# Kernel tuning notes

Measured on AMD Instinct MI355X. Metric: run time of the kernel, lower is better.

Reference implementation:

```python
import jax, jax.numpy as jnp
import numpy as np

ALPHA = 0.2  # LeakyReLU negative slope

def setup_inputs() -> dict:
    key = jax.random.key(0)
    k1, k2, k3 = jax.random.split(key, 3)
    B, N, Fin, Fout = 8, 2048, 256, 128
    h = jax.random.normal(k1, (B, N, Fin), dtype=jnp.float32)
    W = jax.random.normal(k2, (Fin, Fout), dtype=jnp.float32) * (1.414 / np.sqrt(Fin))
    a = jax.random.normal(k3, (2 * Fout, 1), dtype=jnp.float32) * 0.1
    return {"h": h, "W": W, "a": a}

def reference(h, W, a):
    # Wh: [B, N, D]
    Wh = jnp.einsum('bni,io->bno', h, W)
    D = Wh.shape[-1]
    a1 = a[:D, 0]   # weights for the 'i' (repeat_interleave) half
    a2 = a[D:, 0]   # weights for the 'j' (repeat) half
    s1 = Wh @ a1    # [B, N]
    s2 = Wh @ a2    # [B, N]
    # e[b,i,j] = leakyrelu(s1[b,i] + s2[b,j])  (fused form of the O(N^2*2D) concat)
    e = s1[:, :, None] + s2[:, None, :]
    e = jnp.where(e >= 0, e, ALPHA * e)
    # original applies softmax over dim=1 (the i axis)
    attention = jax.nn.softmax(e, axis=1)
    # dropout is identity in eval mode
    h_prime = jnp.einsum('bij,bjd->bid', attention, Wh)
    # concat=True -> ELU
    return jax.nn.elu(h_prime)
```

## Files before the change

### kernel.cpp

```cpp
#include <hip/hip_runtime.h>
#include <hip/hip_bf16.h>


#define ALPHA 0.2f
#define LOG2E 1.4426950408889634f
constexpr int Bb=8, Nn=2048, FIN=256, FOUT=128;

typedef __attribute__((ext_vector_type(8))) short short8;
typedef __attribute__((ext_vector_type(4))) float f32x4;
typedef const __attribute__((address_space(1))) unsigned int* gptr_t;
typedef __attribute__((address_space(3))) unsigned int* lptr_t;

__device__ __forceinline__ float lrelu(float x){ return fmaxf(x, ALPHA*x); }
__device__ __forceinline__ unsigned short bfbits(float x){
    __hip_bfloat16 h = __float2bfloat16(x);
    return *(unsigned short*)&h;
}

__global__ __launch_bounds__(256) void k_prep(const float* __restrict__ W,
                                              __hip_bfloat16* __restrict__ WTt){
    const int idx = blockIdx.x*256 + threadIdx.x;
    #pragma unroll
    for (int v = 0; v < 4; ++v){
        const int widx = idx + v*8192;
        const int kk = widx & 31, n = (widx>>5)&127, kt = widx>>12;
        WTt[widx] = __float2bfloat16(W[(kt*32+kk)*FOUT + n]);
    }
}

__global__ __launch_bounds__(256) void k_wh(const float* __restrict__ h,
                                            const float* __restrict__ a,
                                            const __hip_bfloat16* __restrict__ WTt,
                                            float* __restrict__ s1,
                                            float* __restrict__ s2,
                                            __hip_bfloat16* __restrict__ WhT){
    const int blk = blockIdx.x;
    const int rowbase = blk * 32;
    const int b = blk >> 6;
    const int jt = (rowbase & (Nn-1)) >> 5;
    const int t = threadIdx.x;
    const int wave = t>>6, lane = t&63;
    const int wm = wave & 1, wn = wave >> 1;
    const int lm = lane & 15, q = lane >> 4;

    __shared__ __align__(16) float hs[32*260];
    __shared__ unsigned short tt[FOUT*40];
    __shared__ float s1red[2][32], s2red[2][32];

    {
        const float* srcbase = h + (size_t)rowbase*FIN;
        #pragma unroll
        for (int c = 0; c < 8; ++c){
            const int row = wave*8 + c;
            __builtin_amdgcn_global_load_lds(
                (gptr_t)(srcbase + (size_t)row*FIN + lane*4),
                (lptr_t)&hs[row*260], 16, 0, 0);
        }
    }
    __syncthreads();

    f32x4 acc[4];
    #pragma unroll
    for (int ntl = 0; ntl < 4; ++ntl) acc[ntl] = (f32x4){0.f,0.f,0.f,0.f};

    const float* hrow = &hs[(wm*16 + lm)*260];
    const short* Wt = (const short*)WTt;
    #pragma unroll
    for (int kt = 0; kt < 8; ++kt){
        float av[8];
        *(float4*)&av[0] = *(const float4*)&hrow[kt*32 + q*8];
        *(float4*)&av[4] = *(const float4*)&hrow[kt*32 + q*8 + 4];
        short8 afr;
        #pragma unroll
        for (int e = 0; e < 8; ++e) afr[e] = (short)bfbits(av[e]);
        #pragma unroll
        for (int ntl = 0; ntl < 4; ++ntl){
            const short8 bfr = *(const short8*)(Wt + ((kt*128 + wn*64 + ntl*16 + lm)*32 + q*8));
            acc[ntl] = __builtin_amdgcn_mfma_f32_16x16x32_bf16(afr, bfr, acc[ntl], 0,0,0);
        }
    }

    {
        float a1v[4], a2v[4];
        #pragma unroll
        for (int ntl = 0; ntl < 4; ++ntl){
            a1v[ntl] = a[wn*64 + ntl*16 + lm];
            a2v[ntl] = a[FOUT + wn*64 + ntl*16 + lm];
        }
        #pragma unroll
        for (int rg = 0; rg < 4; ++rg){
            float p1 = 0.f, p2 = 0.f;
            #pragma unroll
            for (int ntl = 0; ntl < 4; ++ntl){
                p1 += acc[ntl][rg]*a1v[ntl];
                p2 += acc[ntl][rg]*a2v[ntl];
            }
            #pragma unroll
            for (int m = 1; m < 16; m <<= 1){
                p1 += __shfl_xor(p1, m);
                p2 += __shfl_xor(p2, m);
            }
            if (lm == 0){
                s1red[wn][wm*16 + q*4 + rg] = p1;
                s2red[wn][wm*16 + q*4 + rg] = p2;
            }
        }
    }

    #pragma unroll
    for (int ntl = 0; ntl < 4; ++ntl){
        ushort4 u;
        u.x = bfbits(acc[ntl][0]); u.y = bfbits(acc[ntl][1]);
        u.z = bfbits(acc[ntl][2]); u.w = bfbits(acc[ntl][3]);
        *(ushort4*)&tt[(wn*64 + ntl*16 + lm)*40 + wm*16 + q*4] = u;
    }
    __syncthreads();

    if (t < 32){
        s1[rowbase + t] = (s1red[0][t] + s1red[1][t]) * LOG2E;
        s2[rowbase + t] = (s2red[0][t] + s2red[1][t]) * LOG2E;
    }
    {
        const int d = t >> 1, jh = (t & 1) * 16;
        const unsigned short* src = &tt[d*40 + jh];
        short8 v0 = *(const short8*)src;
        short8 v1 = *(const short8*)(src + 8);
        const int lmw = d & 15, ntw = d >> 4, q0 = (t & 1) * 2;
        const int u0 = (lmw & 7) + 8*(q0*16 + ntw*2 + (lmw >> 3));
        short* Wo = (short*)WhT;
        const size_t tb = ((size_t)(b*64 + jt))*4096;
        *(short8*)&Wo[tb + (size_t)u0*8]       = v0;
        *(short8*)&Wo[tb + (size_t)(u0+128)*8] = v1;
    }
}

__global__ __launch_bounds__(256) void k_z(const float* __restrict__ s1,
                                           const float* __restrict__ s2,
                                           float* __restrict__ l2z){
    const int b  = blockIdx.x >> 6;
    const int jt = blockIdx.x & 63;
    const int t  = threadIdx.x;
    const int jj = t & 31, part = t >> 5;
    const int j  = jt*32 + jj;
    __shared__ float s1s[Nn];
    __shared__ float red[8][33];

    {
        const float4* g = (const float4*)(s1 + (size_t)b*Nn);
        float4* p = (float4*)s1s;
        #pragma unroll
        for (int v0 = 0; v0 < 2; ++v0){ const int v = t + v0*256; p[v] = g[v]; }
    }
    __syncthreads();
    const float s2j = s2[b*Nn + j];
    float sum = 0.f;
    const float4* s4 = (const float4*)&s1s[part*256];
    #pragma unroll 4
    for (int v = 0; v < 64; ++v){
        float x[4]; *(float4*)x = s4[v];
        sum += __builtin_amdgcn_exp2f(lrelu(x[0]+s2j))
             + __builtin_amdgcn_exp2f(lrelu(x[1]+s2j))
             + __builtin_amdgcn_exp2f(lrelu(x[2]+s2j))
             + __builtin_amdgcn_exp2f(lrelu(x[3]+s2j));
    }
    red[part][jj] = sum;
    __syncthreads();
    if (part == 0){
        float Z = 0.f;
        #pragma unroll
        for (int p = 0; p < 8; ++p) Z += red[p][jj];
        l2z[b*Nn + j] = -__builtin_amdgcn_logf(Z);
    }
}

__global__ __launch_bounds__(256, 2) void k_pv(const float* __restrict__ s1,
                                               const float* __restrict__ s2,
                                               const float* __restrict__ l2z,
                                               const __hip_bfloat16* __restrict__ WhT,
                                               float* __restrict__ out){
    const int blk   = blockIdx.x;
    const int b     = blk & 7;
    const int ibase = (blk >> 3) * 32;
    const int t     = threadIdx.x;
    const int wave  = t >> 6, lane = t & 63;
    const int wm = wave & 1, kh = wave >> 1;
    const int lm = lane & 15, q = lane >> 4;

    __shared__ float s2s[Nn], lzs[Nn];
    __shared__ unsigned short Bs[2][2][8192];

    {
        const float4* g1 = (const float4*)(s2  + (size_t)b*Nn);
        const float4* g2 = (const float4*)(l2z + (size_t)b*Nn);
        float4* p1 = (float4*)s2s; float4* p2 = (float4*)lzs;
        #pragma unroll
        for (int v0 = 0; v0 < 2; ++v0){
            const int v = t + v0*256;
            p1[v] = g1[v]; p2[v] = g2[v];
        }
    }

    const float s1a = s1[(size_t)b*Nn + ibase + wm*16 + lm];

    f32x4 acc[8];
    #pragma unroll
    for (int nt = 0; nt < 8; ++nt) acc[nt] = (f32x4){0.f,0.f,0.f,0.f};

    const char* WtbB = (const char*)WhT + (size_t)b*64*8192;
    const int laneoff = wm*8192 + lane*16;
    const int dsbase  = (lm & 7)*16 + (lm >> 3)*128 + q*2048;

    {
        const char* src = WtbB + (size_t)(kh*16)*16384 + laneoff;
        unsigned short* dst = &Bs[0][kh][wm*4096];
        #pragma unroll
        for (int c = 0; c < 8; ++c)
            __builtin_amdgcn_global_load_lds((gptr_t)(src + c*1024),
                                             (lptr_t)(dst + c*512), 16, 0, 0);
    }

    int buf = 0;
    for (int it = 0; it < 16; ++it){
        __syncthreads();
        if (it + 1 < 16){
            const char* src = WtbB + (size_t)(kh*16 + it + 1)*16384 + laneoff;
            unsigned short* dst = &Bs[buf^1][kh][wm*4096];
            #pragma unroll
            for (int c = 0; c < 8; ++c)
                __builtin_amdgcn_global_load_lds((gptr_t)(src + c*1024),
                                                 (lptr_t)(dst + c*512), 16, 0, 0);
        }
        #pragma unroll
        for (int s = 0; s < 2; ++s){
            const char* tile = (const char*)&Bs[buf][kh][s*4096];
            short8 bfr[8];
            #pragma unroll
            for (int nt = 0; nt < 8; ++nt)
                bfr[nt] = *(const short8*)(tile + dsbase + nt*256);

            const int jb = (kh*16 + it)*64 + s*32 + q*8;
            float sarr[8], larr[8];
            *(float4*)&sarr[0] = *(const float4*)&s2s[jb];
            *(float4*)&sarr[4] = *(const float4*)&s2s[jb+4];
            *(float4*)&larr[0] = *(const float4*)&lzs[jb];
            *(float4*)&larr[4] = *(const float4*)&lzs[jb+4];
            short8 afa;
            #pragma unroll
            for (int e = 0; e < 8; ++e){
                const float z = s1a + sarr[e];
                afa[e] = (short)bfbits(__builtin_amdgcn_exp2f(fmaxf(z, ALPHA*z) + larr[e]));
            }
            #pragma unroll
            for (int nt = 0; nt < 8; ++nt)
                acc[nt] = __builtin_amdgcn_mfma_f32_16x16x32_bf16(afa, bfr[nt], acc[nt], 0,0,0);
        }
        buf ^= 1;
    }

    __syncthreads();
    float* comb = (float*)&Bs[0][0][0];
    if (kh == 0){
        #pragma unroll
        for (int nt = 0; nt < 8; ++nt)
            #pragma unroll
            for (int rg = 0; rg < 4; ++rg)
                comb[(wm*16 + q*4 + rg)*132 + nt*16 + lm] = acc[nt][rg];
    }
    __syncthreads();
    if (kh == 1){
        #pragma unroll
        for (int nt = 0; nt < 8; ++nt){
            const int col = nt*16 + lm;
            #pragma unroll
            for (int rg = 0; rg < 4; ++rg){
                const int row = wm*16 + q*4 + rg;
                const float x = acc[nt][rg] + comb[row*132 + col];
                out[((size_t)(b*Nn + ibase + row))*FOUT + col] = x > 0.f ? x : expm1f(x);
            }
        }
    }
}

extern "C" void kernel_launch(void* const* d_in, const int* in_sizes, int n_in,
                              void* d_out, int out_size, void* d_ws, size_t ws_size,
                              hipStream_t stream) {
    (void)in_sizes; (void)n_in; (void)out_size; (void)ws_size;
    const float* h = (const float*)d_in[0];
    const float* W = (const float*)d_in[1];
    const float* a = (const float*)d_in[2];
    float* out = (float*)d_out;

    float* ws    = (float*)d_ws;
    float* s1    = ws;
    float* s2    = s1 + Bb*Nn;
    float* l2z   = s2 + Bb*Nn;
    __hip_bfloat16* WTt = (__hip_bfloat16*)(l2z + Bb*Nn);
    __hip_bfloat16* WhT = WTt + 32768;

    k_prep<<<dim3(32),        dim3(256), 0, stream>>>(W, WTt);
    k_wh  <<<dim3(Bb*Nn/32),  dim3(256), 0, stream>>>(h, a, WTt, s1, s2, WhT);
    k_z   <<<dim3(Bb*64),     dim3(256), 0, stream>>>(s1, s2, l2z);
    k_pv  <<<dim3(Bb*Nn/32),  dim3(256), 0, stream>>>(s1, s2, l2z, WhT, out);
}
```

Baseline: 103.9 us.

## Switch attention-PV kernel to 32x32x16 MFMA with larger row tiles

Rewrites the final P·V kernel to use 32x32x16 bf16 MFMA instead of 16x16x32. Each block now covers 64 rows with 512 threads and a 4-way K split, and k_wh writes WhT in a matching swizzled layout. The aim is to compute fewer exponentials per useful FLOP, since each exp result feeds a bigger MFMA, and to load WhT tiles less often across blocks. The cost is a three-stage LDS reduction across the four K-split waves, larger shared memory use, and half as many blocks, which may lower occupancy.

New measurement: 100.1 us, median of 2. -3.7%, faster.

```diff
diff --git a/kernel.cpp b/kernel.cpp
--- a/kernel.cpp
+++ b/kernel.cpp
@@ -8,6 +8,7 @@
 
 typedef __attribute__((ext_vector_type(8))) short short8;
 typedef __attribute__((ext_vector_type(4))) float f32x4;
+typedef __attribute__((ext_vector_type(16))) float f32x16;
 typedef const __attribute__((address_space(1))) unsigned int* gptr_t;
 typedef __attribute__((address_space(3))) unsigned int* lptr_t;
 
@@ -121,16 +122,17 @@
         s2[rowbase + t] = (s2red[0][t] + s2red[1][t]) * LOG2E;
     }
     {
-        const int d = t >> 1, jh = (t & 1) * 16;
-        const unsigned short* src = &tt[d*40 + jh];
+        const int d = t >> 1, jsub16 = t & 1;
+        const unsigned short* src = &tt[d*40 + jsub16*16];
         short8 v0 = *(const short8*)src;
         short8 v1 = *(const short8*)(src + 8);
-        const int lmw = d & 15, ntw = d >> 4, q0 = (t & 1) * 2;
-        const int u0 = (lmw & 7) + 8*(q0*16 + ntw*2 + (lmw >> 3));
+        const int s  = (jt & 1)*2 + jsub16;
+        const int nt = d >> 5, col = d & 31;
+        const int u0 = (s*4 + nt)*64 + col;
         short* Wo = (short*)WhT;
-        const size_t tb = ((size_t)(b*64 + jt))*4096;
-        *(short8*)&Wo[tb + (size_t)u0*8]       = v0;
-        *(short8*)&Wo[tb + (size_t)(u0+128)*8] = v1;
+        const size_t tb = ((size_t)(b*32 + (jt >> 1)))*8192;
+        *(short8*)&Wo[tb + (size_t)u0*8]      = v0;
+        *(short8*)&Wo[tb + (size_t)(u0+32)*8] = v1;
     }
 }
 
@@ -173,46 +175,43 @@
     }
 }
 
-__global__ __launch_bounds__(256, 2) void k_pv(const float* __restrict__ s1,
+__global__ __launch_bounds__(512, 2) void k_pv(const float* __restrict__ s1,
                                                const float* __restrict__ s2,
                                                const float* __restrict__ l2z,
                                                const __hip_bfloat16* __restrict__ WhT,
                                                float* __restrict__ out){
     const int blk   = blockIdx.x;
     const int b     = blk & 7;
-    const int ibase = (blk >> 3) * 32;
+    const int ibase = (blk >> 3) * 64;
     const int t     = threadIdx.x;
     const int wave  = t >> 6, lane = t & 63;
-    const int wm = wave & 1, kh = wave >> 1;
-    const int lm = lane & 15, q = lane >> 4;
+    const int wr = wave & 1, kh = wave >> 1;
+    const int il = lane & 31, l5 = lane >> 5;
 
     __shared__ float s2s[Nn], lzs[Nn];
-    __shared__ unsigned short Bs[2][2][8192];
+    __shared__ unsigned short Bs[2][4][8192];
 
     {
         const float4* g1 = (const float4*)(s2  + (size_t)b*Nn);
         const float4* g2 = (const float4*)(l2z + (size_t)b*Nn);
-        float4* p1 = (float4*)s2s; float4* p2 = (float4*)lzs;
-        #pragma unroll
-        for (int v0 = 0; v0 < 2; ++v0){
-            const int v = t + v0*256;
-            p1[v] = g1[v]; p2[v] = g2[v];
-        }
-    }
-
-    const float s1a = s1[(size_t)b*Nn + ibase + wm*16 + lm];
-
-    f32x4 acc[8];
-    #pragma unroll
-    for (int nt = 0; nt < 8; ++nt) acc[nt] = (f32x4){0.f,0.f,0.f,0.f};
-
-    const char* WtbB = (const char*)WhT + (size_t)b*64*8192;
-    const int laneoff = wm*8192 + lane*16;
-    const int dsbase  = (lm & 7)*16 + (lm >> 3)*128 + q*2048;
-
-    {
-        const char* src = WtbB + (size_t)(kh*16)*16384 + laneoff;
-        unsigned short* dst = &Bs[0][kh][wm*4096];
+        ((float4*)s2s)[t] = g1[t];
+        ((float4*)lzs)[t] = g2[t];
+    }
+
+    const float s1a = s1[(size_t)b*Nn + ibase + wr*32 + il];
+
+    f32x16 acc[4];
+    #pragma unroll
+    for (int nt = 0; nt < 4; ++nt)
+        #pragma unroll
+        for (int e = 0; e < 16; ++e) acc[nt][e] = 0.f;
+
+    const char* Wtb = (const char*)WhT + (size_t)b*32*16384;
+    const int laneoff = wr*8192 + lane*16;
+
+    {
+        const char* src = Wtb + (size_t)(kh*8)*16384 + laneoff;
+        unsigned short* dst = &Bs[0][kh][wr*4096];
         #pragma unroll
         for (int c = 0; c < 8; ++c)
             __builtin_amdgcn_global_load_lds((gptr_t)(src + c*1024),
@@ -220,25 +219,25 @@
     }
 
     int buf = 0;
-    for (int it = 0; it < 16; ++it){
+    for (int it = 0; it < 8; ++it){
         __syncthreads();
-        if (it + 1 < 16){
-            const char* src = WtbB + (size_t)(kh*16 + it + 1)*16384 + laneoff;
-            unsigned short* dst = &Bs[buf^1][kh][wm*4096];
+        if (it + 1 < 8){
+            const char* src = Wtb + (size_t)(kh*8 + it + 1)*16384 + laneoff;
+            unsigned short* dst = &Bs[buf^1][kh][wr*4096];
             #pragma unroll
             for (int c = 0; c < 8; ++c)
                 __builtin_amdgcn_global_load_lds((gptr_t)(src + c*1024),
                                                  (lptr_t)(dst + c*512), 16, 0, 0);
         }
-        #pragma unroll
-        for (int s = 0; s < 2; ++s){
-            const char* tile = (const char*)&Bs[buf][kh][s*4096];
-            short8 bfr[8];
-            #pragma unroll
-            for (int nt = 0; nt < 8; ++nt)
-                bfr[nt] = *(const short8*)(tile + dsbase + nt*256);
-
-            const int jb = (kh*16 + it)*64 + s*32 + q*8;
+        const char* tile = (const char*)&Bs[buf][kh][0];
+        #pragma unroll
+        for (int s = 0; s < 4; ++s){
+            short8 bfr[4];
+            #pragma unroll
+            for (int nt = 0; nt < 4; ++nt)
+                bfr[nt] = *(const short8*)(tile + ((s*4 + nt)*64 + lane)*16);
+
+            const int jb = kh*512 + it*64 + s*16 + l5*8;
             float sarr[8], larr[8];
             *(float4*)&sarr[0] = *(const float4*)&s2s[jb];
             *(float4*)&sarr[4] = *(const float4*)&s2s[jb+4];
@@ -251,32 +250,52 @@
                 afa[e] = (short)bfbits(__builtin_amdgcn_exp2f(fmaxf(z, ALPHA*z) + larr[e]));
             }
             #pragma unroll
-            for (int nt = 0; nt < 8; ++nt)
-                acc[nt] = __builtin_amdgcn_mfma_f32_16x16x32_bf16(afa, bfr[nt], acc[nt], 0,0,0);
+            for (int nt = 0; nt < 4; ++nt)
+                acc[nt] = __builtin_amdgcn_mfma_f32_32x32x16_bf16(afa, bfr[nt], acc[nt], 0,0,0);
         }
         buf ^= 1;
     }
 
     __syncthreads();
     float* comb = (float*)&Bs[0][0][0];
-    if (kh == 0){
-        #pragma unroll
-        for (int nt = 0; nt < 8; ++nt)
-            #pragma unroll
-            for (int rg = 0; rg < 4; ++rg)
-                comb[(wm*16 + q*4 + rg)*132 + nt*16 + lm] = acc[nt][rg];
-    }
-    __syncthreads();
-    if (kh == 1){
-        #pragma unroll
-        for (int nt = 0; nt < 8; ++nt){
-            const int col = nt*16 + lm;
-            #pragma unroll
-            for (int rg = 0; rg < 4; ++rg){
-                const int row = wm*16 + q*4 + rg;
-                const float x = acc[nt][rg] + comb[row*132 + col];
-                out[((size_t)(b*Nn + ibase + row))*FOUT + col] = x > 0.f ? x : expm1f(x);
-            }
+    if (kh < 2){
+        float* cb = comb + (size_t)(kh*2 + wr)*(32*132);
+        #pragma unroll
+        for (int nt = 0; nt < 4; ++nt)
+            #pragma unroll
+            for (int r = 0; r < 16; ++r){
+                const int row = (r&3) + 8*(r>>2) + 4*l5;
+                cb[row*132 + nt*32 + il] = acc[nt][r];
+            }
+    }
+    __syncthreads();
+    if (kh >= 2){
+        float* cb = comb + (size_t)((kh-2)*2 + wr)*(32*132);
+        #pragma unroll
+        for (int nt = 0; nt < 4; ++nt)
+            #pragma unroll
+            for (int r = 0; r < 16; ++r){
+                const int row = (r&3) + 8*(r>>2) + 4*l5;
+                cb[row*132 + nt*32 + il] += acc[nt][r];
+            }
+    }
+    __syncthreads();
+    {
+        const int rgrp = t >> 5, c4 = (t & 31)*4;
+        #pragma unroll
+        for (int rr = 0; rr < 4; ++rr){
+            const int row = rgrp*4 + rr;
+            const int wrr = row >> 5, rin = row & 31;
+            const float* r0 = comb + (size_t)(wrr)*(32*132)       + rin*132 + c4;
+            const float* r1 = comb + (size_t)(2 + wrr)*(32*132)   + rin*132 + c4;
+            float4 v0 = *(const float4*)r0, v1 = *(const float4*)r1;
+            float o[4];
+            #pragma unroll
+            for (int e = 0; e < 4; ++e){
+                const float x = ((const float*)&v0)[e] + ((const float*)&v1)[e];
+                o[e] = x > 0.f ? x : expm1f(x);
+            }
+            *(float4*)&out[((size_t)(b*Nn + ibase + row))*FOUT + c4] = *(float4*)o;
         }
     }
 }
@@ -300,5 +319,5 @@
     k_prep<<<dim3(32),        dim3(256), 0, stream>>>(W, WTt);
     k_wh  <<<dim3(Bb*Nn/32),  dim3(256), 0, stream>>>(h, a, WTt, s1, s2, WhT);
     k_z   <<<dim3(Bb*64),     dim3(256), 0, stream>>>(s1, s2, l2z);
-    k_pv  <<<dim3(Bb*Nn/32),  dim3(256), 0, stream>>>(s1, s2, l2z, WhT, out);
-}
+    k_pv  <<<dim3(Bb*Nn/64),  dim3(512), 0, stream>>>(s1, s2, l2z, WhT, out);
+}
```
